# Performance work log

Measured on AMD Instinct MI355X. Metric: run time of the kernel, lower is better.

## Reference

```python
import jax, jax.numpy as jnp
import numpy as np

NEG = -1e30  # stand-in for -inf that keeps logaddexp grad-safe


def _ctc_neg_log_likelihood(predictions, labels):
    # predictions: [B, T, C] logits; labels: [B, L] int, -1 = padding.
    # tf.nn.ctc_loss(blank_index=-1) => blank class is C-1.
    B, T, C = predictions.shape
    L = labels.shape[1]
    S = 2 * L + 1
    blank = C - 1

    label_len = jnp.sum((labels != -1).astype(jnp.int32), axis=-1)  # [B]
    labels_c = jnp.where(labels < 0, 0, labels).astype(jnp.int32)

    # Extended label sequence: blank, l1, blank, l2, ..., blank  -> [B, S]
    ext = jnp.full((B, S), blank, dtype=jnp.int32)
    ext = ext.at[:, 1::2].set(labels_c)

    # s-2 transition allowed only at label positions (odd s) with ext[s] != ext[s-2]
    same = jnp.concatenate([jnp.zeros((B, 2), bool), ext[:, 2:] == ext[:, :-2]], axis=1)
    is_label_pos = (jnp.arange(S) % 2 == 1)[None, :]
    allow2 = is_label_pos & ~same  # [B, S]

    # valid extended positions per example: s < 2*label_len + 1
    valid = jnp.arange(S)[None, :] < (2 * label_len + 1)[:, None]  # [B, S]

    log_probs = jax.nn.log_softmax(predictions, axis=-1)  # [B, T, C]
    # emission log-prob for each extended-label slot: [B, T, S]
    lp_ext = jnp.take_along_axis(log_probs, jnp.broadcast_to(ext[:, None, :], (B, T, S)), axis=2)

    has_lab = label_len > 0
    alpha0 = jnp.full((B, S), NEG, dtype=log_probs.dtype)
    alpha0 = alpha0.at[:, 0].set(lp_ext[:, 0, 0])
    alpha0 = alpha0.at[:, 1].set(jnp.where(has_lab, lp_ext[:, 0, 1], NEG))
    alpha0 = jnp.where(valid, alpha0, NEG)

    def step(alpha, lp_t):
        a1 = alpha
        a2 = jnp.pad(alpha, ((0, 0), (1, 0)), constant_values=NEG)[:, :S]
        a3 = jnp.pad(alpha, ((0, 0), (2, 0)), constant_values=NEG)[:, :S]
        a3 = jnp.where(allow2, a3, NEG)
        new = jnp.logaddexp(jnp.logaddexp(a1, a2), a3) + lp_t
        new = jnp.where(valid, new, NEG)
        return new, None

    lp_rest = jnp.moveaxis(lp_ext[:, 1:], 1, 0)  # [T-1, B, S]
    alphaT, _ = jax.lax.scan(step, alpha0, lp_rest)

    idx1 = (2 * label_len)[:, None]              # final blank
    idx2 = jnp.maximum(idx1 - 1, 0)              # final label
    a_end1 = jnp.take_along_axis(alphaT, idx1, axis=1)[:, 0]
    a_end2 = jnp.take_along_axis(alphaT, idx2, axis=1)[:, 0]
    a_end2 = jnp.where(has_lab, a_end2, NEG)
    log_lik = jnp.logaddexp(a_end1, a_end2)
    return -log_lik  # [B]


def setup_inputs() -> dict:
    key = jax.random.key(0)
    k1, k2 = jax.random.split(key)
    B, T, C, L = 1024, 384, 96, 48
    labels = jax.random.randint(k1, (B, L), 0, C - 1).astype(jnp.int64)
    predictions = jax.random.normal(k2, (B, T, C), dtype=jnp.float32)
    return {"labels": labels, "predictions": predictions}


def reference(labels, predictions):
    per_example = _ctc_neg_log_likelihood(predictions, labels)
    return jnp.mean(per_example)
```

## Files before the change

kernel.cpp:

```cpp
#include <hip/hip_runtime.h>

constexpr int Tt = 384;
constexpr int Cc = 96;
constexpr int Ll = 48;
constexpr int Gg = 8;
constexpr int NG = 24;

#define L2E 1.4426950408889634f
#define LN2 0.6931471805599453f
#define LNEG (-3.0e38f)

template <int CTRL, int RM = 0xF>
__device__ __forceinline__ float dppf(float x) {
    return __int_as_float(
        __builtin_amdgcn_update_dpp(0, __float_as_int(x), CTRL, RM, 0xF, true));
}
template <int CTRL>
__device__ __forceinline__ int dppi(int x) {
    return __builtin_amdgcn_update_dpp(0, x, CTRL, 0xF, 0xF, true);
}
__device__ __forceinline__ float bcast63(float x) {
    return __int_as_float(__builtin_amdgcn_readlane(__float_as_int(x), 63));
}
__device__ __forceinline__ float wsum(float x) {
    x += dppf<0x111>(x);
    x += dppf<0x112>(x);
    x += dppf<0x114>(x);
    x += dppf<0x118>(x);
    x += dppf<0x142, 0xA>(x);
    x += dppf<0x143, 0xC>(x);
    return bcast63(x);
}
__device__ __forceinline__ float shup1(float x) { return dppf<0x138>(x); }
__device__ __forceinline__ float shdn1(float x) { return dppf<0x130>(x); }
__device__ __forceinline__ float exp2i(int d) {
    d = d < -126 ? -126 : (d > 126 ? 126 : d);
    return __int_as_float((d + 127) << 23);
}

template <bool FWD>
__device__ __forceinline__ void prod_load(const float2* __restrict__ rp2, float2* q,
                                          int g, int lane) {
#pragma unroll
    for (int j = 0; j < Gg; ++j) {
        int k = g * Gg + j;
        int t = FWD ? k : (Tt - 1 - k);
        q[j] = (lane < 48) ? rp2[(size_t)t * 48 + lane] : make_float2(-1e4f, -1e4f);
    }
}
__device__ __forceinline__ void prod_group(const float2* q, float* dst, int lane,
                                           int idx_h, int bitsel) {
#pragma unroll
    for (int j = 0; j < Gg; ++j) {
        float ex = exp2f(q[j].x * L2E);
        float ey = exp2f(q[j].y * L2E);
        float s  = (lane < 48) ? (ex + ey) : 0.0f;
        float gb = __shfl(ey, 47, 64);
        float g0 = __shfl(ex, idx_h, 64);
        float g1 = __shfl(ey, idx_h, 64);
        s = wsum(s);
        float rZ = __builtin_amdgcn_rcpf(s);
        float pl = (bitsel ? g1 : g0) * rZ;
        float pb = gb * rZ;
        dst[j * 64 + lane] = (lane == 49) ? pb : pl;
    }
}

template <bool FWD>
__device__ __forceinline__ void dp_group(const float* __restrict__ pr, int lane,
                                         float allow2f, float& st_e, float& st_o,
                                         int& ls, float& f, float& a2f) {
    float plC[Gg], pbC[Gg];
#pragma unroll
    for (int j = 0; j < Gg; ++j) {
        plC[j] = pr[j * 64 + lane];
        pbC[j] = pr[j * 64 + 49];
    }
#pragma unroll
    for (int j = 0; j < Gg; ++j) {
        if (FWD) {
            float sh = shup1(st_o);
            float t0 = st_e + st_o;
            float ne = fmaf(f, sh, st_e) * pbC[j];
            float no = fmaf(a2f, sh, t0) * plC[j];
            st_e = ne; st_o = no;
        } else {
            float en = shdn1(st_e);
            float on = shdn1(st_o);
            float ne = (st_e + st_o) * pbC[j];
            float no = fmaf(a2f, on, fmaf(f, en, st_o)) * plC[j];
            st_e = ne; st_o = no;
        }
    }
    float m = fmaxf(st_e, st_o);
    bool z  = (m == 0.0f);
    int eb  = (__float_as_int(m) >> 23) & 0xFF;
    eb = eb > 253 ? 253 : eb;
    float r = z ? 1.0f : __int_as_float((254 - eb) << 23);
    st_e *= r; st_o *= r;
    ls += z ? 0 : (eb - 127);
#pragma unroll
    for (int it = 0; it < 8; ++it) {
        int lsn = FWD ? dppi<0x138>(ls) : dppi<0x130>(ls);
        ls = z ? lsn : ls;
    }
    int lsn2 = FWD ? dppi<0x138>(ls) : dppi<0x130>(ls);
    f   = exp2i(lsn2 - ls);
    a2f = allow2f * f;
}

__global__ __launch_bounds__(64) void zero_kernel(float* o) { *o = 0.0f; }

__global__ __launch_bounds__(256) void ctc_fb(const int* __restrict__ labels,
                                              const float* __restrict__ pred,
                                              float* __restrict__ out,
                                              float invB) {
    const int b    = blockIdx.x;
    const int lane = threadIdx.x & 63;
    const int wv   = threadIdx.x >> 6;
    const float2* rp2 = (const float2*)(pred + (size_t)b * Tt * Cc);

    __shared__ float plb[2][2][Gg][64];
    __shared__ float sbe[64], sbo[64];
    __shared__ int   slsb[64];

    int v = (lane < Ll) ? labels[(size_t)b * Ll + lane] : -1;
    int present = (lane < Ll) && (v != -1);
    int labv = (v < 0) ? 0 : v;
    unsigned long long pm = __ballot(present);
    int len = __popcll(pm);
    int idx_h  = labv >> 1;
    int bitsel = labv & 1;
    int lab_p = __shfl(labv, (lane - 1) & 63, 64);
    int lab_n = __shfl(labv, (lane + 1) & 63, 64);

    float st_e = 0.0f, st_o = 0.0f, f = 1.0f, a2f = 0.0f, allow2f = 0.0f;
    int   ls = 0;
    float2 qA[Gg], qB[Gg];

    if (wv == 0) {
        allow2f = (lane >= 1 && labv != lab_p) ? 1.0f : 0.0f;
        st_e = (lane == 0) ? 1.0f : 0.0f;
        a2f = allow2f;
    } else if (wv == 1) {
        allow2f = (labv != lab_n) ? 1.0f : 0.0f;
        st_e = (lane == len) ? 1.0f : 0.0f;
        a2f = allow2f;
    } else if (wv == 2) {
        prod_load<true>(rp2, qA, 0, lane);
        prod_load<true>(rp2, qB, 1, lane);
    } else {
        prod_load<false>(rp2, qA, 0, lane);
        prod_load<false>(rp2, qB, 1, lane);
    }

    for (int i = 0; i <= NG; ++i) {
        if (wv == 2 && i < NG) {
            if ((i & 1) == 0) {
                prod_group(qA, &plb[0][0][0][0], lane, idx_h, bitsel);
                if (i + 2 < NG) prod_load<true>(rp2, qA, i + 2, lane);
            } else {
                prod_group(qB, &plb[0][1][0][0], lane, idx_h, bitsel);
                if (i + 2 < NG) prod_load<true>(rp2, qB, i + 2, lane);
            }
        } else if (wv == 3 && i < NG) {
            if ((i & 1) == 0) {
                prod_group(qA, &plb[1][0][0][0], lane, idx_h, bitsel);
                if (i + 2 < NG) prod_load<false>(rp2, qA, i + 2, lane);
            } else {
                prod_group(qB, &plb[1][1][0][0], lane, idx_h, bitsel);
                if (i + 2 < NG) prod_load<false>(rp2, qB, i + 2, lane);
            }
        } else if (wv == 0 && i >= 1) {
            dp_group<true>(&plb[0][(i - 1) & 1][0][0], lane, allow2f, st_e, st_o, ls, f, a2f);
        } else if (wv == 1 && i >= 1) {
            dp_group<false>(&plb[1][(i - 1) & 1][0][0], lane, allow2f, st_e, st_o, ls, f, a2f);
        }
        __syncthreads();
    }

    if (wv == 1) {
        sbe[lane]  = st_e;
        sbo[lane]  = st_o;
        slsb[lane] = ls;
    }
    __syncthreads();

    if (wv == 0) {
        float sh  = shup1(st_o);
        int   lsu = dppi<0x138>(ls);
        float fup = exp2i(lsu - ls);
        float Ae = fmaf(fup, sh, st_e);
        float Ao = fmaf(allow2f * fup, sh, st_e + st_o);
        float be = sbe[lane], bo = sbo[lane];
        float base = (float)(ls + slsb[lane]);
        float l1 = (Ae > 0.0f && be > 0.0f) ? __log2f(Ae) + __log2f(be) + base : LNEG;
        float l2 = (Ao > 0.0f && bo > 0.0f) ? __log2f(Ao) + __log2f(bo) + base : LNEG;
        float mm = fmaxf(l1, l2);
#pragma unroll
        for (int off = 32; off >= 1; off >>= 1) mm = fmaxf(mm, __shfl_xor(mm, off, 64));
        float ss = exp2f(l1 - mm) + exp2f(l2 - mm);
#pragma unroll
        for (int off = 32; off >= 1; off >>= 1) ss += __shfl_xor(ss, off, 64);
        if (lane == 0) {
            float ll = (mm + __log2f(ss)) * LN2;
            atomicAdd(out, -ll * invB);
        }
    }
}

extern "C" void kernel_launch(void* const* d_in, const int* in_sizes, int n_in,
                              void* d_out, int out_size, void* d_ws, size_t ws_size,
                              hipStream_t stream) {
    const int*   labels = (const int*)d_in[0];
    const float* pred   = (const float*)d_in[1];
    float*       out    = (float*)d_out;

    const int B = in_sizes[0] / Ll;

    hipLaunchKernelGGL(zero_kernel, dim3(1), dim3(64), 0, stream, out);
    hipLaunchKernelGGL(ctc_fb, dim3(B), dim3(256), 0, stream,
                       labels, pred, out, 1.0f / (float)B);
}
```

Before: 225.6 us.

## Precompute all emission probabilities in parallel before the serial forward-backward DP

The producer/consumer pipeline with a block barrier per group is replaced by a two-phase scheme. Eight waves first compute the softmax-gathered emission probabilities for the whole sequence in both directions into compact shared memory (row stride 50). Two waves then run the forward and backward recursions without any per-group barrier. This spreads the exp/softmax work over more waves and removes 25 block-wide syncs, but uses about 77 KB of shared memory per block and serialises loading before the DP starts.

```diff
diff --git a/kernel.cpp b/kernel.cpp
--- a/kernel.cpp
+++ b/kernel.cpp
@@ -5,6 +5,10 @@
 constexpr int Ll = 48;
 constexpr int Gg = 8;
 constexpr int NG = 24;
+constexpr int GPW = 6;
+constexpr int RS = 50;
+constexpr int DSZ = NG * Gg * RS;
+constexpr int PAD = 16;
 
 #define L2E 1.4426950408889634f
 #define LN2 0.6931471805599453f
@@ -38,31 +42,30 @@
     return __int_as_float((d + 127) << 23);
 }
 
-template <bool FWD>
-__device__ __forceinline__ void prod_load(const float2* __restrict__ rp2, float2* q,
-                                          int g, int lane) {
+__device__ __forceinline__ void load_group(const float2* __restrict__ rp2, float2* q,
+                                           int dir, int g, int lane) {
 #pragma unroll
     for (int j = 0; j < Gg; ++j) {
         int k = g * Gg + j;
-        int t = FWD ? k : (Tt - 1 - k);
+        int t = dir ? (Tt - 1 - k) : k;
         q[j] = (lane < 48) ? rp2[(size_t)t * 48 + lane] : make_float2(-1e4f, -1e4f);
     }
 }
-__device__ __forceinline__ void prod_group(const float2* q, float* dst, int lane,
-                                           int idx_h, int bitsel) {
-#pragma unroll
-    for (int j = 0; j < Gg; ++j) {
-        float ex = exp2f(q[j].x * L2E);
-        float ey = exp2f(q[j].y * L2E);
-        float s  = (lane < 48) ? (ex + ey) : 0.0f;
+
+__device__ __forceinline__ void sm_store(const float2* q, float* dst, int lane,
+                                         int idx_h, int bitsel) {
+#pragma unroll
+    for (int j = 0; j < Gg; ++j) {
+        float ex = __builtin_amdgcn_exp2f(q[j].x * L2E);
+        float ey = __builtin_amdgcn_exp2f(q[j].y * L2E);
         float gb = __shfl(ey, 47, 64);
         float g0 = __shfl(ex, idx_h, 64);
         float g1 = __shfl(ey, idx_h, 64);
-        s = wsum(s);
+        float s  = wsum(ex + ey);
         float rZ = __builtin_amdgcn_rcpf(s);
         float pl = (bitsel ? g1 : g0) * rZ;
         float pb = gb * rZ;
-        dst[j * 64 + lane] = (lane == 49) ? pb : pl;
+        if (lane < RS) dst[j * RS + lane] = (lane == 49) ? pb : pl;
     }
 }
 
@@ -73,8 +76,8 @@
     float plC[Gg], pbC[Gg];
 #pragma unroll
     for (int j = 0; j < Gg; ++j) {
-        plC[j] = pr[j * 64 + lane];
-        pbC[j] = pr[j * 64 + 49];
+        plC[j] = pr[j * RS + lane];
+        pbC[j] = pr[j * RS + 49];
     }
 #pragma unroll
     for (int j = 0; j < Gg; ++j) {
@@ -111,16 +114,16 @@
 
 __global__ __launch_bounds__(64) void zero_kernel(float* o) { *o = 0.0f; }
 
-__global__ __launch_bounds__(256) void ctc_fb(const int* __restrict__ labels,
-                                              const float* __restrict__ pred,
-                                              float* __restrict__ out,
-                                              float invB) {
+__global__ __launch_bounds__(512, 4) void ctc_fb(const int* __restrict__ labels,
+                                                 const float* __restrict__ pred,
+                                                 float* __restrict__ out,
+                                                 float invB) {
     const int b    = blockIdx.x;
     const int lane = threadIdx.x & 63;
     const int wv   = threadIdx.x >> 6;
     const float2* rp2 = (const float2*)(pred + (size_t)b * Tt * Cc);
 
-    __shared__ float plb[2][2][Gg][64];
+    __shared__ float plb[2][DSZ + PAD];
     __shared__ float sbe[64], sbo[64];
     __shared__ int   slsb[64];
 
@@ -134,52 +137,45 @@
     int lab_p = __shfl(labv, (lane - 1) & 63, 64);
     int lab_n = __shfl(labv, (lane + 1) & 63, 64);
 
+    if (threadIdx.x < 2 * PAD) {
+        int d = threadIdx.x / PAD, i = threadIdx.x % PAD;
+        plb[d][DSZ + i] = 0.0f;
+    }
+
+    {
+        const int ag0 = GPW * wv;
+        const int dir = (ag0 >= NG) ? 1 : 0;
+        const int g0  = ag0 - dir * NG;
+        float2 q0[Gg], q1[Gg];
+        load_group(rp2, q0, dir, g0 + 0, lane);
+        load_group(rp2, q1, dir, g0 + 1, lane);
+#pragma unroll
+        for (int i = 0; i < GPW; ++i) {
+            if ((i & 1) == 0) {
+                sm_store(q0, &plb[dir][(g0 + i) * Gg * RS], lane, idx_h, bitsel);
+                if (i + 2 < GPW) load_group(rp2, q0, dir, g0 + i + 2, lane);
+            } else {
+                sm_store(q1, &plb[dir][(g0 + i) * Gg * RS], lane, idx_h, bitsel);
+                if (i + 2 < GPW) load_group(rp2, q1, dir, g0 + i + 2, lane);
+            }
+        }
+    }
+    __syncthreads();
+
     float st_e = 0.0f, st_o = 0.0f, f = 1.0f, a2f = 0.0f, allow2f = 0.0f;
     int   ls = 0;
-    float2 qA[Gg], qB[Gg];
-
     if (wv == 0) {
         allow2f = (lane >= 1 && labv != lab_p) ? 1.0f : 0.0f;
         st_e = (lane == 0) ? 1.0f : 0.0f;
         a2f = allow2f;
+        for (int g = 0; g < NG; ++g)
+            dp_group<true>(&plb[0][g * Gg * RS], lane, allow2f, st_e, st_o, ls, f, a2f);
     } else if (wv == 1) {
         allow2f = (labv != lab_n) ? 1.0f : 0.0f;
         st_e = (lane == len) ? 1.0f : 0.0f;
         a2f = allow2f;
-    } else if (wv == 2) {
-        prod_load<true>(rp2, qA, 0, lane);
-        prod_load<true>(rp2, qB, 1, lane);
-    } else {
-        prod_load<false>(rp2, qA, 0, lane);
-        prod_load<false>(rp2, qB, 1, lane);
-    }
-
-    for (int i = 0; i <= NG; ++i) {
-        if (wv == 2 && i < NG) {
-            if ((i & 1) == 0) {
-                prod_group(qA, &plb[0][0][0][0], lane, idx_h, bitsel);
-                if (i + 2 < NG) prod_load<true>(rp2, qA, i + 2, lane);
-            } else {
-                prod_group(qB, &plb[0][1][0][0], lane, idx_h, bitsel);
-                if (i + 2 < NG) prod_load<true>(rp2, qB, i + 2, lane);
-            }
-        } else if (wv == 3 && i < NG) {
-            if ((i & 1) == 0) {
-                prod_group(qA, &plb[1][0][0][0], lane, idx_h, bitsel);
-                if (i + 2 < NG) prod_load<false>(rp2, qA, i + 2, lane);
-            } else {
-                prod_group(qB, &plb[1][1][0][0], lane, idx_h, bitsel);
-                if (i + 2 < NG) prod_load<false>(rp2, qB, i + 2, lane);
-            }
-        } else if (wv == 0 && i >= 1) {
-            dp_group<true>(&plb[0][(i - 1) & 1][0][0], lane, allow2f, st_e, st_o, ls, f, a2f);
-        } else if (wv == 1 && i >= 1) {
-            dp_group<false>(&plb[1][(i - 1) & 1][0][0], lane, allow2f, st_e, st_o, ls, f, a2f);
-        }
-        __syncthreads();
-    }
-
-    if (wv == 1) {
+        for (int g = 0; g < NG; ++g)
+            dp_group<false>(&plb[1][g * Gg * RS], lane, allow2f, st_e, st_o, ls, f, a2f);
         sbe[lane]  = st_e;
         sbo[lane]  = st_o;
         slsb[lane] = ls;
@@ -219,6 +215,6 @@
     const int B = in_sizes[0] / Ll;
 
     hipLaunchKernelGGL(zero_kernel, dim3(1), dim3(64), 0, stream, out);
-    hipLaunchKernelGGL(ctc_fb, dim3(B), dim3(256), 0, stream,
+    hipLaunchKernelGGL(ctc_fb, dim3(B), dim3(512), 0, stream,
                        labels, pred, out, 1.0f / (float)B);
 }
```

After: 240.6 us. +6.6%, slower.
